# Kernel optimization log

Hardware: AMD Instinct MI355X
Metric: run time of the kernel (lower is better)

## Reference

```python
import jax, jax.numpy as jnp
import numpy as np

B, S, DIN, DATTN, DMODEL, M, HEADS, NSYNC, OUT, T, HNLM = 64, 64, 512, 512, 2048, 25, 8, 512, 1000, 50, 32

def _ln(x, g, b, eps=1e-5):
    mu = x.mean(-1, keepdims=True)
    v = x.var(-1, keepdims=True)
    return (x - mu) / jnp.sqrt(v + eps) * g + b

def setup_inputs() -> dict:
    key = jax.random.key(0)
    ks = jax.random.split(key, 32)
    def n(k, shape, fan):
        return jax.random.normal(k, shape, jnp.float32) / jnp.sqrt(jnp.float32(fan))
    inp = {}
    inp['x'] = jax.random.normal(ks[0], (B, S, DIN), jnp.float32)
    inp['Wf'] = n(ks[1], (DIN, DATTN), DIN); inp['bf'] = jnp.zeros((DATTN,), jnp.float32)
    inp['start_trace'] = jax.random.normal(ks[2], (DMODEL, M), jnp.float32) * 0.02
    inp['start_state'] = jax.random.normal(ks[3], (DMODEL,), jnp.float32) * 0.02
    inp['decay_a'] = jax.random.uniform(ks[4], (NSYNC,), jnp.float32, 0.0, 2.0)
    inp['decay_o'] = jax.random.uniform(ks[5], (NSYNC,), jnp.float32, 0.0, 2.0)
    inp['Wqp'] = n(ks[6], (NSYNC, DATTN), NSYNC); inp['bqp'] = jnp.zeros((DATTN,), jnp.float32)
    inp['Wq'] = n(ks[7], (DATTN, DATTN), DATTN); inp['bq'] = jnp.zeros((DATTN,), jnp.float32)
    inp['Wk'] = n(ks[8], (DATTN, DATTN), DATTN); inp['bk'] = jnp.zeros((DATTN,), jnp.float32)
    inp['Wv'] = n(ks[9], (DATTN, DATTN), DATTN); inp['bv'] = jnp.zeros((DATTN,), jnp.float32)
    inp['Wo'] = n(ks[10], (DATTN, DATTN), DATTN); inp['bo'] = jnp.zeros((DATTN,), jnp.float32)
    inp['Ws1'] = n(ks[11], (DATTN + DMODEL, 2 * DMODEL), DATTN + DMODEL); inp['bs1'] = jnp.zeros((2 * DMODEL,), jnp.float32)
    inp['ln_g'] = jnp.ones((DMODEL,), jnp.float32); inp['ln_b'] = jnp.zeros((DMODEL,), jnp.float32)
    inp['nw1'] = n(ks[12], (DMODEL, M, HNLM), M); inp['nb1'] = jnp.zeros((DMODEL, HNLM), jnp.float32)
    inp['nw2'] = n(ks[13], (DMODEL, HNLM), HNLM); inp['nb2'] = jnp.zeros((DMODEL,), jnp.float32)
    inp['Wout'] = n(ks[14], (NSYNC, OUT), NSYNC); inp['bout'] = jnp.zeros((OUT,), jnp.float32)
    inp['idx_la'] = jax.random.randint(ks[15], (NSYNC,), 0, DMODEL)
    inp['idx_ra'] = jax.random.randint(ks[16], (NSYNC,), 0, DMODEL)
    inp['idx_lo'] = jax.random.randint(ks[17], (NSYNC,), 0, DMODEL)
    inp['idx_ro'] = jax.random.randint(ks[18], (NSYNC,), 0, DMODEL)
    return inp

def _forward(x, Wf, bf, start_trace, start_state, decay_a, decay_o, Wqp, bqp, Wq, bq, Wk, bk, Wv, bv, Wo, bo, Ws1, bs1, ln_g, ln_b, nw1, nb1, nw2, nb2, Wout, bout, idx_la, idx_ra, idx_lo, idx_ro):
    Bn = x.shape[0]
    hd = DATTN // HEADS
    kv = x @ Wf + bf                                     # (B,S,DATTN)
    K = (kv @ Wk + bk).reshape(Bn, S, HEADS, hd)         # static across ticks
    V = (kv @ Wv + bv).reshape(Bn, S, HEADS, hd)
    r_a = jnp.exp(-jnp.clip(decay_a, 0.0, 15.0))
    r_o = jnp.exp(-jnp.clip(decay_o, 0.0, 15.0))
    trace0 = jnp.broadcast_to(start_trace[None], (Bn, DMODEL, M))
    act0 = jnp.broadcast_to(start_state[None], (Bn, DMODEL))

    def sync(state, alpha, beta, r, il, ir):
        pairing = state[:, il] * state[:, ir]
        alpha = r[None] * alpha + pairing
        beta = r[None] * beta + 1.0
        return alpha / jnp.sqrt(beta), alpha, beta

    # initial 'out' synchronisation (alpha=None/beta=None path)
    aO0 = act0[:, idx_lo] * act0[:, idx_ro]
    bO0 = jnp.ones_like(aO0)
    aA0 = jnp.zeros((Bn, NSYNC), jnp.float32)
    bA0 = jnp.zeros((Bn, NSYNC), jnp.float32)

    def step(carry, _):
        trace, act, aA, bA, aO, bO = carry
        syA, aA, bA = sync(act, aA, bA, r_a, idx_la, idx_ra)
        q = syA @ Wqp + bqp                              # (B,DATTN)
        Qh = (q @ Wq + bq).reshape(Bn, HEADS, hd)
        sc = jnp.einsum('bhd,bshd->bhs', Qh, K) / jnp.sqrt(jnp.float32(hd))
        w = jax.nn.softmax(sc, -1)
        ao = jnp.einsum('bhs,bshd->bhd', w, V).reshape(Bn, DATTN) @ Wo + bo
        pre = jnp.concatenate([ao, act], -1)             # (B,DATTN+DMODEL)
        h = pre @ Ws1 + bs1
        a1, a2 = jnp.split(h, 2, -1)
        state = _ln(a1 * jax.nn.sigmoid(a2), ln_g, ln_b) # GLU -> LayerNorm
        trace = jnp.concatenate([trace[:, :, 1:], state[:, :, None]], -1)
        hn = jax.nn.gelu(jnp.einsum('bdm,dmh->bdh', trace, nw1) + nb1)
        act = jnp.einsum('bdh,dh->bd', hn, nw2) + nb2    # neuron-level models
        syO, aO, bO = sync(act, aO, bO, r_o, idx_lo, idx_ro)
        pred = syO @ Wout + bout
        logp = jax.nn.log_softmax(pred, -1)
        ne = -(jnp.exp(logp) * logp).sum(-1) / jnp.log(jnp.float32(OUT))
        cert = jnp.stack([ne, 1.0 - ne], -1)
        return (trace, act, aA, bA, aO, bO), (pred, cert, syO)

    _, (preds, certs, syOs) = jax.lax.scan(step, (trace0, act0, aA0, bA0, aO0, bO0), None, length=T)
    predictions = jnp.moveaxis(preds, 0, -1)             # (B,OUT,T)
    certainties = jnp.moveaxis(certs, 0, -1)             # (B,2,T)
    return predictions, certainties, syOs[-1]

def reference(x, Wf, bf, start_trace, start_state, decay_a, decay_o, Wqp, bqp, Wq, bq, Wk, bk, Wv, bv, Wo, bo, Ws1, bs1, ln_g, ln_b, nw1, nb1, nw2, nb2, Wout, bout, idx_la, idx_ra, idx_lo, idx_ro):
    return _forward(x, Wf, bf, start_trace, start_state, decay_a, decay_o, Wqp, bqp, Wq, bq, Wk, bk, Wv, bv, Wo, bo, Ws1, bs1, ln_g, ln_b, nw1, nb1, nw2, nb2, Wout, bout, idx_la, idx_ra, idx_lo, idx_ro)
```

## Files before the change

### kernel.cpp

```cpp
#include <hip/hip_runtime.h>
#include <hip/hip_bf16.h>
#include <math.h>

#define BB 64
#define SS 64
#define DA 512
#define DM 2048
#define MM 25
#define NH 8
#define HD 64
#define NS 512
#define NOUT 1000
#define TT 50
#define HN 32
#define KTOT 2560
#define NOUT2 4096
#define KCH 640
#define NPAD 1024
#define SB2 ((size_t)BB*NS)

typedef __attribute__((ext_vector_type(8))) short bf16x8_t;
typedef __attribute__((ext_vector_type(8))) unsigned short u16x8_t;
typedef __attribute__((ext_vector_type(4))) float f32x4_t;

__device__ inline float bfs2f(unsigned short u){
    unsigned int x = ((unsigned int)u) << 16;
    return __uint_as_float(x);
}
__device__ inline unsigned short f2bfu(float v){
    __hip_bfloat16 h = __float2bfloat16(v);
    return *reinterpret_cast<unsigned short*>(&h);
}
__device__ inline float gelu_tanh(float x){
    float x3 = x*x*x;
    float u = 0.7978845608028654f*(x + 0.044715f*x3);
    float eu = __expf(2.f*u);
    float th = 1.f - 2.f/(eu + 1.f);
    return 0.5f*x*(1.0f + th);
}

static const size_t OFF_K     = 0;
static const size_t OFF_V     = OFF_K     + (size_t)BB*SS*DA/2;
static const size_t OFF_WCT   = OFF_V     + (size_t)BB*SS*DA/2;
static const size_t OFF_WC1   = OFF_WCT   + (size_t)NOUT2*KTOT/2;
static const size_t OFF_WOUTT = OFF_WC1   + (size_t)DA*DA;
static const size_t OFF_NW1B  = OFF_WOUTT + (size_t)NPAD*NS/2;
static const size_t OFF_WFK   = OFF_NW1B  + (size_t)DM*MM*HN/2;
static const size_t OFF_WFV   = OFF_WFK   + (size_t)DA*DA;
static const size_t OFF_BFK   = OFF_WFV   + (size_t)DA*DA;
static const size_t OFF_BFV   = OFF_BFK   + DA;
static const size_t OFF_BC1   = OFF_BFV   + DA;
static const size_t OFF_BC2   = OFF_BC1   + DA;
static const size_t OFF_BOUTP = OFF_BC2   + 2*DM;
static const size_t OFF_AA    = OFF_BOUTP + NPAD;
static const size_t OFF_BA    = OFF_AA    + 2*SB2;
static const size_t OFF_AO    = OFF_BA    + 2*SB2;
static const size_t OFF_BO    = OFF_AO    + 2*SB2;
static const size_t OFF_ATT   = OFF_BO    + 2*SB2;
static const size_t OFF_ACTB  = OFF_ATT   + (size_t)BB*DA/2;
static const size_t OFF_ACTF  = OFF_ACTB  + (size_t)BB*DM/2;
static const size_t OFF_HP    = OFF_ACTF  + (size_t)DM*BB;
static const size_t OFF_SBUF  = OFF_HP    + (size_t)4*BB*2*DM;
static const size_t OFF_STATS = OFF_SBUF  + (size_t)BB*DM;
static const size_t OFF_TRB   = OFF_STATS + 128;
static const size_t OFF_PREDA = OFF_TRB   + (size_t)MM*DM*BB/2;
static const size_t OFF_END   = OFF_PREDA + (size_t)TT*BB*NPAD/2;

__global__ void sgemm64(const float* __restrict__ A, int lda,
                        const float* __restrict__ Bm, int ldb,
                        const float* __restrict__ bias,
                        float* __restrict__ C, int ldc, int Kdim)
{
    __shared__ float la[16][65];
    __shared__ float lb[16][64];
    int cg = blockIdx.x, rg = blockIdx.y, tid = threadIdx.x;
    int tx = tid & 15, ty = tid >> 4;
    const float* Ab = A + (size_t)rg*64*lda;
    const float* Bb = Bm + (size_t)cg*64;
    float acc[4][4] = {};
    for (int k0 = 0; k0 < Kdim; k0 += 16){
        for (int i = tid; i < 1024; i += 256){
            int r = i >> 4, kk = i & 15;
            la[kk][r] = Ab[(size_t)r*lda + k0 + kk];
        }
        for (int i = tid; i < 1024; i += 256){
            int kk = i >> 6, c = i & 63;
            lb[kk][c] = Bb[(size_t)(k0+kk)*ldb + c];
        }
        __syncthreads();
        #pragma unroll
        for (int kk = 0; kk < 16; ++kk){
            float av[4], bv[4];
            #pragma unroll
            for (int i = 0; i < 4; ++i) av[i] = la[kk][ty*4+i];
            #pragma unroll
            for (int j = 0; j < 4; ++j) bv[j] = lb[kk][tx*4+j];
            #pragma unroll
            for (int i = 0; i < 4; ++i)
                #pragma unroll
                for (int j = 0; j < 4; ++j) acc[i][j] += av[i]*bv[j];
        }
        __syncthreads();
    }
    for (int i = 0; i < 4; ++i){
        int row = rg*64 + ty*4 + i;
        for (int j = 0; j < 4; ++j){
            int col = cg*64 + tx*4 + j;
            float v = acc[i][j];
            if (bias) v += bias[col];
            C[(size_t)row*ldc + col] = v;
        }
    }
}

__global__ void sgemm64_bf16out(const float* __restrict__ A, int lda,
                                const float* __restrict__ Bm, int ldb,
                                const float* __restrict__ bias,
                                unsigned short* __restrict__ C, int ldc, int Kdim)
{
    __shared__ float la[16][65];
    __shared__ float lb[16][64];
    int cg = blockIdx.x, rg = blockIdx.y, tid = threadIdx.x;
    int tx = tid & 15, ty = tid >> 4;
    const float* Ab = A + (size_t)rg*64*lda;
    const float* Bb = Bm + (size_t)cg*64;
    float acc[4][4] = {};
    for (int k0 = 0; k0 < Kdim; k0 += 16){
        for (int i = tid; i < 1024; i += 256){
            int r = i >> 4, kk = i & 15;
            la[kk][r] = Ab[(size_t)r*lda + k0 + kk];
        }
        for (int i = tid; i < 1024; i += 256){
            int kk = i >> 6, c = i & 63;
            lb[kk][c] = Bb[(size_t)(k0+kk)*ldb + c];
        }
        __syncthreads();
        #pragma unroll
        for (int kk = 0; kk < 16; ++kk){
            float av[4], bv[4];
            #pragma unroll
            for (int i = 0; i < 4; ++i) av[i] = la[kk][ty*4+i];
            #pragma unroll
            for (int j = 0; j < 4; ++j) bv[j] = lb[kk][tx*4+j];
            #pragma unroll
            for (int i = 0; i < 4; ++i)
                #pragma unroll
                for (int j = 0; j < 4; ++j) acc[i][j] += av[i]*bv[j];
        }
        __syncthreads();
    }
    for (int i = 0; i < 4; ++i){
        int row = rg*64 + ty*4 + i;
        for (int j = 0; j < 4; ++j){
            int col = cg*64 + tx*4 + j;
            float v = acc[i][j];
            if (bias) v += bias[col];
            C[(size_t)row*ldc + col] = f2bfu(v);
        }
    }
}

__global__ void gemm_t_bf16(const float* __restrict__ A, const float* __restrict__ Bm,
                            int ldb, unsigned short* __restrict__ Ct, int ldct)
{
    __shared__ float la[16][65];
    __shared__ float lb[16][64];
    int cg = blockIdx.x, rg = blockIdx.y, tid = threadIdx.x;
    int tx = tid & 15, ty = tid >> 4;
    const float* Ab = A + (size_t)rg*64*512;
    const float* Bb = Bm + (size_t)cg*64;
    float acc[4][4] = {};
    for (int k0 = 0; k0 < 512; k0 += 16){
        for (int i = tid; i < 1024; i += 256){
            int r = i >> 4, kk = i & 15;
            la[kk][r] = Ab[(size_t)r*512 + k0 + kk];
        }
        for (int i = tid; i < 1024; i += 256){
            int kk = i >> 6, c = i & 63;
            lb[kk][c] = Bb[(size_t)(k0+kk)*ldb + c];
        }
        __syncthreads();
        #pragma unroll
        for (int kk = 0; kk < 16; ++kk){
            float av[4], bv[4];
            #pragma unroll
            for (int i = 0; i < 4; ++i) av[i] = la[kk][ty*4+i];
            #pragma unroll
            for (int j = 0; j < 4; ++j) bv[j] = lb[kk][tx*4+j];
            #pragma unroll
            for (int i = 0; i < 4; ++i)
                #pragma unroll
                for (int j = 0; j < 4; ++j) acc[i][j] += av[i]*bv[j];
        }
        __syncthreads();
    }
    for (int i = 0; i < 4; ++i){
        int krow = rg*64 + ty*4 + i;
        for (int j = 0; j < 4; ++j){
            int ncol = cg*64 + tx*4 + j;
            Ct[(size_t)ncol*ldct + krow] = f2bfu(acc[i][j]);
        }
    }
}

__global__ void tcvt_ws1(const float* __restrict__ Ws1, unsigned short* __restrict__ WcT)
{
    __shared__ float tile[32][33];
    int bx = blockIdx.x, by = blockIdx.y;
    int tx = threadIdx.x & 31, ty = threadIdx.x >> 5;
    for (int i = 0; i < 4; ++i){
        int r = by*32 + ty + i*8;
        tile[ty + i*8][tx] = Ws1[(size_t)(512 + r)*NOUT2 + bx*32 + tx];
    }
    __syncthreads();
    for (int i = 0; i < 4; ++i){
        int n = bx*32 + ty + i*8;
        int r = by*32 + tx;
        WcT[(size_t)n*KTOT + 512 + r] = f2bfu(tile[tx][ty + i*8]);
    }
}

__global__ void tcvt_wout(const float* __restrict__ Wout, const float* __restrict__ bout,
                          unsigned short* __restrict__ WoutT, float* __restrict__ boutp)
{
    int n = blockIdx.x;
    int tid = threadIdx.x;
    for (int k = tid; k < NS; k += 256)
        WoutT[(size_t)n*NS + k] = (n < NOUT) ? f2bfu(Wout[(size_t)k*NOUT + n]) : (unsigned short)0;
    if (tid == 0) boutp[n] = (n < NOUT) ? bout[n] : 0.f;
}

__global__ void bias_combo(const float* __restrict__ bvec, const float* __restrict__ W,
                           int ldw, const float* __restrict__ badd,
                           float* __restrict__ out, int N)
{
    int n = blockIdx.x*256 + threadIdx.x;
    if (n >= N) return;
    float acc = badd[n];
    for (int k = 0; k < 512; ++k) acc += bvec[k]*W[(size_t)k*ldw + n];
    out[n] = acc;
}

__global__ void cvt_bf16(const float* __restrict__ in, unsigned short* __restrict__ out, int n)
{
    int i = blockIdx.x*256 + threadIdx.x;
    if (i < n) out[i] = f2bfu(in[i]);
}

__global__ void init_state(const float* __restrict__ ss,
                           const int* __restrict__ ilo, const int* __restrict__ iro,
                           float* __restrict__ act_f, unsigned short* __restrict__ act_bf,
                           float* __restrict__ aA0, float* __restrict__ bA0,
                           float* __restrict__ aO0, float* __restrict__ bO0)
{
    int i = blockIdx.x*256 + threadIdx.x;
    if (i < BB*DM){
        int d = i >> 6, b = i & 63;
        float v = ss[d];
        act_f[(size_t)d*BB + b] = v;
        act_bf[(size_t)b*DM + d] = f2bfu(v);
    }
    if (i < BB*NS){
        int j = i & (NS-1);
        aA0[i] = 0.f; bA0[i] = 0.f;
        aO0[i] = ss[ilo[j]]*ss[iro[j]];
        bO0[i] = 1.f;
    }
}

__device__ void pred_body(char* smem, int pb,
                          const float* __restrict__ act_f,
                          float* __restrict__ aO, float* __restrict__ bO,
                          const int* __restrict__ ilo, const int* __restrict__ iro,
                          const float* __restrict__ dco,
                          const unsigned short* __restrict__ WoutT,
                          const float* __restrict__ boutp,
                          unsigned short* __restrict__ predA,
                          float* __restrict__ out_syo, int tp)
{
    unsigned short* Asy = (unsigned short*)smem;
    const int tid = threadIdx.x, lane = tid & 63, w = tid >> 6;
    const int rf = w & 3, cf2 = (w >> 2)*2;
    const int colb = lane & 15, koff = (lane >> 4)*8, rg4 = (lane >> 4)*4;
    const int n0 = pb*64;
    const int rdn = tp & 1, wrn = 1 - rdn;
    f32x4_t acc0 = {0.f,0.f,0.f,0.f}, acc1 = {0.f,0.f,0.f,0.f};
    for (int ks = 0; ks < 8; ++ks){
        int jj = tid & 63, bq = tid >> 6;
        int j = ks*64 + jj;
        int ilj = ilo[j], irj = iro[j];
        float rr = __expf(-fminf(fmaxf(dco[j], 0.f), 15.f));
        #pragma unroll
        for (int p = 0; p < 8; ++p){
            int b = p*8 + bq;
            float pair = act_f[(size_t)ilj*BB + b]*act_f[(size_t)irj*BB + b];
            size_t o = (size_t)b*NS + j;
            float a  = rr*aO[(size_t)rdn*SB2 + o] + pair;
            float be = rr*bO[(size_t)rdn*SB2 + o] + 1.f;
            float s = a*rsqrtf(be);
            Asy[b*72 + jj] = f2bfu(s);
            if (pb == 0){
                aO[(size_t)wrn*SB2 + o] = a;
                bO[(size_t)wrn*SB2 + o] = be;
                if (tp == TT-1) out_syo[o] = s;
            }
        }
        __syncthreads();
        int arow = rf*16 + colb;
        bf16x8_t a0 = *(const bf16x8_t*)&Asy[arow*72 + koff];
        bf16x8_t a1 = *(const bf16x8_t*)&Asy[arow*72 + 32 + koff];
        int br0 = n0 + cf2*16 + colb, br1 = br0 + 16;
        bf16x8_t b00 = *(const bf16x8_t*)&WoutT[(size_t)br0*NS + ks*64 + koff];
        bf16x8_t b01 = *(const bf16x8_t*)&WoutT[(size_t)br0*NS + ks*64 + 32 + koff];
        bf16x8_t b10 = *(const bf16x8_t*)&WoutT[(size_t)br1*NS + ks*64 + koff];
        bf16x8_t b11 = *(const bf16x8_t*)&WoutT[(size_t)br1*NS + ks*64 + 32 + koff];
        acc0 = __builtin_amdgcn_mfma_f32_16x16x32_bf16(a0, b00, acc0, 0, 0, 0);
        acc0 = __builtin_amdgcn_mfma_f32_16x16x32_bf16(a1, b01, acc0, 0, 0, 0);
        acc1 = __builtin_amdgcn_mfma_f32_16x16x32_bf16(a0, b10, acc1, 0, 0, 0);
        acc1 = __builtin_amdgcn_mfma_f32_16x16x32_bf16(a1, b11, acc1, 0, 0, 0);
        __syncthreads();
    }
    unsigned short* pa = predA + (size_t)tp*BB*NPAD;
    #pragma unroll
    for (int r = 0; r < 4; ++r){
        int row = rf*16 + rg4 + r;
        int c0 = n0 + cf2*16 + colb, c1 = c0 + 16;
        pa[(size_t)row*NPAD + c0] = f2bfu(acc0[r] + boutp[c0]);
        pa[(size_t)row*NPAD + c1] = f2bfu(acc1[r] + boutp[c1]);
    }
}

__global__ __launch_bounds__(512) void tick_head(
        const float* __restrict__ act_f,
        float* __restrict__ aA, float* __restrict__ bA,
        float* __restrict__ aO, float* __restrict__ bO,
        const int* __restrict__ ila, const int* __restrict__ ira,
        const int* __restrict__ ilo, const int* __restrict__ iro,
        const float* __restrict__ dca, const float* __restrict__ dco,
        const float* __restrict__ Wc1, const float* __restrict__ bc1,
        const unsigned short* __restrict__ Kb, const unsigned short* __restrict__ Vb,
        unsigned short* __restrict__ att,
        const unsigned short* __restrict__ WoutT, const float* __restrict__ boutp,
        unsigned short* __restrict__ predA, float* __restrict__ out_syo,
        int t, int do_pred)
{
    __shared__ __align__(16) char smem[20480];
    const int bid = blockIdx.x, tid = threadIdx.x;
    const int lane = tid & 63, w = tid >> 6;
    if (bid < 64){
        int h = bid >> 3, bg = bid & 7;
        float* sy  = (float*)smem;
        float* q   = sy + 8*NS;
        float* wgt = q + 8*64;
        int rdn = t & 1, wrn = 1 - rdn;
        for (int i = tid; i < 8*NS; i += 512){
            int r = i >> 9, j = i & (NS-1);
            int b = bg*8 + r;
            float pair = act_f[(size_t)ila[j]*BB + b]*act_f[(size_t)ira[j]*BB + b];
            float rr = __expf(-fminf(fmaxf(dca[j], 0.f), 15.f));
            size_t o = (size_t)b*NS + j;
            float a  = rr*aA[(size_t)rdn*SB2 + o] + pair;
            float be = rr*bA[(size_t)rdn*SB2 + o] + 1.f;
            sy[i] = a*rsqrtf(be);
            if (h == 0){ aA[(size_t)wrn*SB2 + o] = a; bA[(size_t)wrn*SB2 + o] = be; }
        }
        __syncthreads();
        {
            int c = lane, r = w;
            int col = h*HD + c;
            float acc = bc1[col];
            const float* wp = Wc1 + col;
            #pragma unroll 8
            for (int k = 0; k < NS; ++k) acc += sy[r*NS + k]*wp[(size_t)k*DA];
            q[r*64 + c] = acc;
        }
        __syncthreads();
        {
            int r = w, s = lane;
            int b = bg*8 + r;
            const unsigned short* kp = Kb + (size_t)(b*SS + s)*DA + h*HD;
            float sc = 0.f;
            #pragma unroll
            for (int dg = 0; dg < 8; ++dg){
                u16x8_t kv = *(const u16x8_t*)(kp + dg*8);
                #pragma unroll
                for (int u = 0; u < 8; ++u) sc += q[r*64 + dg*8 + u]*bfs2f(kv[u]);
            }
            sc *= 0.125f;
            float m = sc;
            for (int o = 32; o; o >>= 1) m = fmaxf(m, __shfl_xor(m, o, 64));
            float e = __expf(sc - m);
            float sum = e;
            for (int o = 32; o; o >>= 1) sum += __shfl_xor(sum, o, 64);
            wgt[r*64 + s] = e/sum;
        }
        __syncthreads();
        {
            int r = w, d = lane;
            int b = bg*8 + r;
            const unsigned short* vp = Vb + (size_t)(b*SS)*DA + h*HD + d;
            float o = 0.f;
            #pragma unroll 8
            for (int s = 0; s < SS; ++s) o += wgt[r*64 + s]*bfs2f(vp[(size_t)s*DA]);
            att[(size_t)b*DA + h*HD + d] = f2bfu(o);
        }
    } else if (do_pred){
        pred_body(smem, bid - 64, act_f, aO, bO, ilo, iro, dco,
                  WoutT, boutp, predA, out_syo, t - 1);
    }
}

__global__ __launch_bounds__(512) void pred_fin(
        const float* __restrict__ act_f,
        float* __restrict__ aO, float* __restrict__ bO,
        const int* __restrict__ ilo, const int* __restrict__ iro,
        const float* __restrict__ dco,
        const unsigned short* __restrict__ WoutT, const float* __restrict__ boutp,
        unsigned short* __restrict__ predA, float* __restrict__ out_syo)
{
    __shared__ __align__(16) char smem[10240];
    pred_body(smem, blockIdx.x, act_f, aO, bO, ilo, iro, dco,
              WoutT, boutp, predA, out_syo, TT - 1);
}

__global__ __launch_bounds__(256) void hgemm_mfma(const unsigned short* __restrict__ attu,
                                                  const unsigned short* __restrict__ actu,
                                                  const unsigned short* __restrict__ wctu,
                                                  float* __restrict__ hpart)
{
    __shared__ unsigned short Al[64][72];
    __shared__ unsigned short Bl[64][72];
    int cg = blockIdx.x, kc = blockIdx.y, tid = threadIdx.x;
    int w = tid >> 6, lane = tid & 63;
    int n0 = cg*64;
    f32x4_t acc[4];
    #pragma unroll
    for (int t2 = 0; t2 < 4; ++t2) acc[t2] = (f32x4_t){0.f,0.f,0.f,0.f};

    for (int step = 0; step < 10; ++step){
        int k0 = kc*KCH + step*64;
        #pragma unroll
        for (int ld = 0; ld < 2; ++ld){
            int idx = tid + ld*256;
            int row = idx >> 3;
            int kg  = (idx & 7)*8;
            *reinterpret_cast<uint4*>(&Bl[row][kg]) =
                *reinterpret_cast<const uint4*>(&wctu[(size_t)(n0+row)*KTOT + k0 + kg]);
            uint4 av;
            if (k0 < 512) av = *reinterpret_cast<const uint4*>(&attu[(size_t)row*DA + k0 + kg]);
            else          av = *reinterpret_cast<const uint4*>(&actu[(size_t)row*DM + (k0-512) + kg]);
            *reinterpret_cast<uint4*>(&Al[row][kg]) = av;
        }
        __syncthreads();
        int arow = w*16 + (lane & 15);
        int koff = (lane >> 4)*8;
        bf16x8_t af0 = *reinterpret_cast<const bf16x8_t*>(&Al[arow][koff]);
        bf16x8_t af1 = *reinterpret_cast<const bf16x8_t*>(&Al[arow][32 + koff]);
        #pragma unroll
        for (int t2 = 0; t2 < 4; ++t2){
            int brow = t2*16 + (lane & 15);
            bf16x8_t bf0 = *reinterpret_cast<const bf16x8_t*>(&Bl[brow][koff]);
            bf16x8_t bf1 = *reinterpret_cast<const bf16x8_t*>(&Bl[brow][32 + koff]);
            acc[t2] = __builtin_amdgcn_mfma_f32_16x16x32_bf16(af0, bf0, acc[t2], 0, 0, 0);
            acc[t2] = __builtin_amdgcn_mfma_f32_16x16x32_bf16(af1, bf1, acc[t2], 0, 0, 0);
        }
        __syncthreads();
    }
    float* out = hpart + (size_t)kc*BB*2*DM;
    int colb = lane & 15, rg2 = (lane >> 4)*4;
    #pragma unroll
    for (int t2 = 0; t2 < 4; ++t2){
        #pragma unroll
        for (int r = 0; r < 4; ++r){
            int row = w*16 + rg2 + r;
            int col = n0 + t2*16 + colb;
            out[(size_t)row*2*DM + col] = acc[t2][r];
        }
    }
}

__global__ void glu_stats(const float* __restrict__ hp, const float* __restrict__ bc2,
                          float* __restrict__ sbuf, float* __restrict__ stats)
{
    __shared__ float red[8];
    int b = blockIdx.x, tid = threadIdx.x;
    int lane = tid & 63, w = tid >> 6;
    float lsum = 0.f, lsq = 0.f;
    #pragma unroll
    for (int i = 0; i < 8; ++i){
        int n = tid + i*256;
        float h1 = bc2[n], h2 = bc2[DM + n];
        #pragma unroll
        for (int c = 0; c < 4; ++c){
            const float* hb = hp + ((size_t)c*BB + b)*2*DM;
            h1 += hb[n]; h2 += hb[DM + n];
        }
        float s = h1*(1.f/(1.f + __expf(-h2)));
        sbuf[(size_t)b*DM + n] = s;
        lsum += s; lsq += s*s;
    }
    for (int o = 32; o; o >>= 1){ lsum += __shfl_down(lsum, o, 64); lsq += __shfl_down(lsq, o, 64); }
    if (lane == 0){ red[w] = lsum; red[4 + w] = lsq; }
    __syncthreads();
    if (tid == 0){
        float ts = red[0]+red[1]+red[2]+red[3];
        float tq = red[4]+red[5]+red[6]+red[7];
        float mu = ts/DM;
        float var = tq/DM - mu*mu;
        stats[b*2] = mu;
        stats[b*2+1] = rsqrtf(var + 1e-5f);
    }
}

__global__ __launch_bounds__(512) void nlm2(
        const float* __restrict__ sbuf, const float* __restrict__ stats,
        const float* __restrict__ lng, const float* __restrict__ lnb,
        unsigned short* __restrict__ traceb, const float* __restrict__ stt,
        const unsigned short* __restrict__ nw1b, const float* __restrict__ nb1,
        const float* __restrict__ nw2, const float* __restrict__ nb2,
        float* __restrict__ act_f, unsigned short* __restrict__ act_bf, int t)
{
    __shared__ float wall[8*864];
    const int tid = threadIdx.x, lane = tid & 63, w = tid >> 6;
    const int d = blockIdx.x*8 + w;
    float* wreg = wall + (size_t)w*864;
    for (int i = lane; i < 800; i += 64) wreg[i] = bfs2f(nw1b[(size_t)d*800 + i]);
    if (lane < 32) wreg[800 + lane] = nb1[d*HN + lane];
    else           wreg[832 + (lane - 32)] = nw2[d*HN + (lane - 32)];
    float mu  = stats[lane*2];
    float inv = stats[lane*2 + 1];
    float s   = sbuf[(size_t)lane*DM + d];
    float st  = (s - mu)*inv*lng[d] + lnb[d];
    int slot = t % MM;
    traceb[((size_t)slot*DM + d)*BB + lane] = f2bfu(st);
    float tr[25];
    #pragma unroll
    for (int m = 0; m < 24; ++m){
        int time = t - 24 + m;
        tr[m] = (time >= 0) ? bfs2f(traceb[((size_t)(time % MM)*DM + d)*BB + lane])
                            : stt[(size_t)d*MM + (m + t + 1)];
    }
    tr[24] = st;
    float a[32];
    #pragma unroll
    for (int h = 0; h < 32; ++h) a[h] = wreg[800 + h];
    #pragma unroll
    for (int m = 0; m < 25; ++m){
        float tm = tr[m];
        #pragma unroll
        for (int q4 = 0; q4 < 8; ++q4){
            float4 w4 = *(const float4*)&wreg[m*32 + q4*4];
            a[q4*4+0] += tm*w4.x;
            a[q4*4+1] += tm*w4.y;
            a[q4*4+2] += tm*w4.z;
            a[q4*4+3] += tm*w4.w;
        }
    }
    float pa = 0.f;
    #pragma unroll
    for (int h = 0; h < 32; ++h) pa += gelu_tanh(a[h])*wreg[832 + h];
    float v = pa + nb2[d];
    act_f[(size_t)d*BB + lane] = v;
    act_bf[(size_t)lane*DM + d] = f2bfu(v);
}

__global__ void entropy_k(const unsigned short* __restrict__ predA, float* __restrict__ out_cert)
{
    __shared__ float red[8];
    int b = blockIdx.x & 63, t = blockIdx.x >> 6, tid = threadIdx.x;
    const unsigned short* pr = predA + (size_t)t*BB*NPAD + (size_t)b*NPAD;
    float v[4];
    float m = -1e30f;
    #pragma unroll
    for (int i = 0; i < 4; ++i){
        int n = tid + i*256;
        v[i] = (n < NOUT) ? bfs2f(pr[n]) : -1e30f;
        m = fmaxf(m, v[i]);
    }
    for (int o = 32; o; o >>= 1) m = fmaxf(m, __shfl_xor(m, o, 64));
    if ((tid & 63) == 0) red[tid >> 6] = m;
    __syncthreads();
    m = fmaxf(fmaxf(red[0], red[1]), fmaxf(red[2], red[3]));
    __syncthreads();
    float s1 = 0.f, s2 = 0.f;
    #pragma unroll
    for (int i = 0; i < 4; ++i){
        int n = tid + i*256;
        if (n < NOUT){
            float e = __expf(v[i] - m);
            s1 += e; s2 += e*(v[i] - m);
        }
    }
    for (int o = 32; o; o >>= 1){ s1 += __shfl_xor(s1, o, 64); s2 += __shfl_xor(s2, o, 64); }
    if ((tid & 63) == 0){ red[tid >> 6] = s1; red[4 + (tid >> 6)] = s2; }
    __syncthreads();
    s1 = red[0]+red[1]+red[2]+red[3];
    s2 = red[4]+red[5]+red[6]+red[7];
    float plogp = s2/s1 - logf(s1);
    float ne = -plogp / logf((float)NOUT);
    if (tid == 0){
        out_cert[(size_t)b*2*TT + t]      = ne;
        out_cert[(size_t)b*2*TT + TT + t] = 1.f - ne;
    }
}

__global__ void transpose_pred(const unsigned short* __restrict__ predA, float* __restrict__ out_pred)
{
    __shared__ unsigned short sm[50][136];
    int bx = blockIdx.x;
    int b  = blockIdx.y;
    int tid = threadIdx.x;
    for (int tp = 0; tp < 25; ++tp){
        int t = tp*2 + (tid >> 7);
        int nn = tid & 127;
        sm[t][nn] = predA[(size_t)t*BB*NPAD + (size_t)b*NPAD + bx*128 + nn];
    }
    __syncthreads();
    int nloc = tid >> 1, half = tid & 1;
    int n = bx*128 + nloc;
    if (n < NOUT){
        float* dst = out_pred + (size_t)b*NOUT*TT + (size_t)n*TT + half*25;
        #pragma unroll
        for (int q = 0; q < 25; ++q) dst[q] = bfs2f(sm[half*25 + q][nloc]);
    }
}

extern "C" void kernel_launch(void* const* d_in, const int* in_sizes, int n_in,
                              void* d_out, int out_size, void* d_ws, size_t ws_size,
                              hipStream_t stream)
{
    const float* x    = (const float*)d_in[0];
    const float* Wf   = (const float*)d_in[1];
    const float* bf   = (const float*)d_in[2];
    const float* stt  = (const float*)d_in[3];
    const float* ss   = (const float*)d_in[4];
    const float* dca  = (const float*)d_in[5];
    const float* dco  = (const float*)d_in[6];
    const float* Wqp  = (const float*)d_in[7];
    const float* bqp  = (const float*)d_in[8];
    const float* Wq   = (const float*)d_in[9];
    const float* bq   = (const float*)d_in[10];
    const float* Wk   = (const float*)d_in[11];
    const float* bk   = (const float*)d_in[12];
    const float* Wv   = (const float*)d_in[13];
    const float* bv   = (const float*)d_in[14];
    const float* Wo   = (const float*)d_in[15];
    const float* bo   = (const float*)d_in[16];
    const float* Ws1  = (const float*)d_in[17];
    const float* bs1  = (const float*)d_in[18];
    const float* lng  = (const float*)d_in[19];
    const float* lnb  = (const float*)d_in[20];
    const float* nw1  = (const float*)d_in[21];
    const float* nb1  = (const float*)d_in[22];
    const float* nw2  = (const float*)d_in[23];
    const float* nb2  = (const float*)d_in[24];
    const float* Wout = (const float*)d_in[25];
    const float* bout = (const float*)d_in[26];
    const int* ila = (const int*)d_in[27];
    const int* ira = (const int*)d_in[28];
    const int* ilo = (const int*)d_in[29];
    const int* iro = (const int*)d_in[30];

    float* ws = (float*)d_ws;
    unsigned short* Kb    = (unsigned short*)(ws + OFF_K);
    unsigned short* Vb    = (unsigned short*)(ws + OFF_V);
    unsigned short* WcT   = (unsigned short*)(ws + OFF_WCT);
    float*          Wc1   = ws + OFF_WC1;
    unsigned short* WoutT = (unsigned short*)(ws + OFF_WOUTT);
    unsigned short* nw1b  = (unsigned short*)(ws + OFF_NW1B);
    float* Wfk   = ws + OFF_WFK;
    float* Wfv   = ws + OFF_WFV;
    float* bfk   = ws + OFF_BFK;
    float* bfv   = ws + OFF_BFV;
    float* bc1   = ws + OFF_BC1;
    float* bc2   = ws + OFF_BC2;
    float* boutp = ws + OFF_BOUTP;
    float* aA    = ws + OFF_AA;
    float* bA    = ws + OFF_BA;
    float* aO    = ws + OFF_AO;
    float* bO    = ws + OFF_BO;
    unsigned short* attb  = (unsigned short*)(ws + OFF_ATT);
    unsigned short* actb  = (unsigned short*)(ws + OFF_ACTB);
    float* actf  = ws + OFF_ACTF;
    float* hp    = ws + OFF_HP;
    float* sbuf  = ws + OFF_SBUF;
    float* stats = ws + OFF_STATS;
    unsigned short* traceb = (unsigned short*)(ws + OFF_TRB);
    unsigned short* predA  = (unsigned short*)(ws + OFF_PREDA);

    float* outp = (float*)d_out;
    float* out_pred = outp;
    float* out_cert = outp + (size_t)BB*NOUT*TT;
    float* out_syo  = out_cert + (size_t)BB*2*TT;

    sgemm64<<<dim3(8,8),  256, 0, stream>>>(Wf, 512, Wk, 512, nullptr, Wfk, 512, 512);
    sgemm64<<<dim3(8,8),  256, 0, stream>>>(Wf, 512, Wv, 512, nullptr, Wfv, 512, 512);
    sgemm64<<<dim3(8,8),  256, 0, stream>>>(Wqp,512, Wq, 512, nullptr, Wc1, 512, 512);
    gemm_t_bf16<<<dim3(64,8), 256, 0, stream>>>(Wo, Ws1, NOUT2, WcT, KTOT);
    tcvt_ws1<<<dim3(128,64), 256, 0, stream>>>(Ws1, WcT);
    tcvt_wout<<<NPAD, 256, 0, stream>>>(Wout, bout, WoutT, boutp);
    bias_combo<<<2, 256, 0, stream>>>(bf,  Wk, 512, bk, bfk, 512);
    bias_combo<<<2, 256, 0, stream>>>(bf,  Wv, 512, bv, bfv, 512);
    bias_combo<<<2, 256, 0, stream>>>(bqp, Wq, 512, bq, bc1, 512);
    bias_combo<<<16,256, 0, stream>>>(bo,  Ws1, NOUT2, bs1, bc2, 4096);
    cvt_bf16<<<6400, 256, 0, stream>>>(nw1, nw1b, DM*MM*HN);
    sgemm64_bf16out<<<dim3(8,64), 256, 0, stream>>>(x, 512, Wfk, 512, bfk, Kb, 512, 512);
    sgemm64_bf16out<<<dim3(8,64), 256, 0, stream>>>(x, 512, Wfv, 512, bfv, Vb, 512, 512);
    init_state<<<512, 256, 0, stream>>>(ss, ilo, iro, actf, actb, aA, bA, aO, bO);

    for (int t = 0; t < TT; ++t){
        tick_head<<<80, 512, 0, stream>>>(actf, aA, bA, aO, bO,
                                          ila, ira, ilo, iro, dca, dco,
                                          Wc1, bc1, Kb, Vb, attb,
                                          WoutT, boutp, predA, out_syo,
                                          t, (t > 0) ? 1 : 0);
        hgemm_mfma<<<dim3(64,4), 256, 0, stream>>>(attb, actb, WcT, hp);
        glu_stats<<<BB, 256, 0, stream>>>(hp, bc2, sbuf, stats);
        nlm2<<<256, 512, 0, stream>>>(sbuf, stats, lng, lnb, traceb, stt,
                                      nw1b, nb1, nw2, nb2, actf, actb, t);
    }
    pred_fin<<<16, 512, 0, stream>>>(actf, aO, bO, ilo, iro, dco,
                                     WoutT, boutp, predA, out_syo);

    entropy_k<<<TT*BB, 256, 0, stream>>>(predA, out_cert);
    transpose_pred<<<dim3(8, BB), 256, 0, stream>>>(predA, out_pred);
}
```

Before: 4.663 ms.

## Fuse GLU and layernorm stats into per-tick GEMM; move setup GEMMs to MFMA

The per-tick split-K GEMM plus separate GLU/stats kernel is replaced by one hgemm_glu kernel. Each block computes 8 paired gate/value columns over the full K, applies the GLU in registers and accumulates row sum and sum-of-squares with atomics. The intent is to drop the partial-sum buffer round-trip and one launch per tick; nlm2 now derives mean and rsqrt itself, and tick_head zeroes the stats. The one-time weight-folding GEMMs are moved to bf16 MFMA with transposed bf16 copies, and Wc1 is stored as bf16. This trades fp32 precision in the precomputation and uses atomics in place of a deterministic reduction.

```diff
diff --git a/kernel.cpp b/kernel.cpp
--- a/kernel.cpp
+++ b/kernel.cpp
@@ -15,7 +15,6 @@
 #define HN 32
 #define KTOT 2560
 #define NOUT2 4096
-#define KCH 640
 #define NPAD 1024
 #define SB2 ((size_t)BB*NS)
 
@@ -40,167 +39,100 @@
 }
 
 static const size_t OFF_K     = 0;
-static const size_t OFF_V     = OFF_K     + (size_t)BB*SS*DA/2;
-static const size_t OFF_WCT   = OFF_V     + (size_t)BB*SS*DA/2;
-static const size_t OFF_WC1   = OFF_WCT   + (size_t)NOUT2*KTOT/2;
-static const size_t OFF_WOUTT = OFF_WC1   + (size_t)DA*DA;
-static const size_t OFF_NW1B  = OFF_WOUTT + (size_t)NPAD*NS/2;
-static const size_t OFF_WFK   = OFF_NW1B  + (size_t)DM*MM*HN/2;
-static const size_t OFF_WFV   = OFF_WFK   + (size_t)DA*DA;
-static const size_t OFF_BFK   = OFF_WFV   + (size_t)DA*DA;
-static const size_t OFF_BFV   = OFF_BFK   + DA;
-static const size_t OFF_BC1   = OFF_BFV   + DA;
-static const size_t OFF_BC2   = OFF_BC1   + DA;
-static const size_t OFF_BOUTP = OFF_BC2   + 2*DM;
-static const size_t OFF_AA    = OFF_BOUTP + NPAD;
+static const size_t OFF_V     = OFF_K     + 1048576;
+static const size_t OFF_WCT   = OFF_V     + 1048576;
+static const size_t OFF_WC1B  = OFF_WCT   + 5242880;
+static const size_t OFF_WOUTT = OFF_WC1B  + 131072;
+static const size_t OFF_NW1B  = OFF_WOUTT + 262144;
+static const size_t OFF_WFT   = OFF_NW1B  + 819200;
+static const size_t OFF_WKT   = OFF_WFT   + 131072;
+static const size_t OFF_WVT   = OFF_WKT   + 131072;
+static const size_t OFF_WQT   = OFF_WVT   + 131072;
+static const size_t OFF_WQPB  = OFF_WQT   + 131072;
+static const size_t OFF_WOB   = OFF_WQPB  + 131072;
+static const size_t OFF_BC1   = OFF_WOB   + 131072;
+static const size_t OFF_BC2   = OFF_BC1   + 512;
+static const size_t OFF_BOUTP = OFF_BC2   + 4096;
+static const size_t OFF_AA    = OFF_BOUTP + 1024;
 static const size_t OFF_BA    = OFF_AA    + 2*SB2;
 static const size_t OFF_AO    = OFF_BA    + 2*SB2;
 static const size_t OFF_BO    = OFF_AO    + 2*SB2;
 static const size_t OFF_ATT   = OFF_BO    + 2*SB2;
-static const size_t OFF_ACTB  = OFF_ATT   + (size_t)BB*DA/2;
-static const size_t OFF_ACTF  = OFF_ACTB  + (size_t)BB*DM/2;
-static const size_t OFF_HP    = OFF_ACTF  + (size_t)DM*BB;
-static const size_t OFF_SBUF  = OFF_HP    + (size_t)4*BB*2*DM;
-static const size_t OFF_STATS = OFF_SBUF  + (size_t)BB*DM;
+static const size_t OFF_ACTB  = OFF_ATT   + 16384;
+static const size_t OFF_ACTF  = OFF_ACTB  + 65536;
+static const size_t OFF_SBUF  = OFF_ACTF  + 131072;
+static const size_t OFF_STATS = OFF_SBUF  + 131072;
 static const size_t OFF_TRB   = OFF_STATS + 128;
-static const size_t OFF_PREDA = OFF_TRB   + (size_t)MM*DM*BB/2;
-static const size_t OFF_END   = OFF_PREDA + (size_t)TT*BB*NPAD/2;
-
-__global__ void sgemm64(const float* __restrict__ A, int lda,
-                        const float* __restrict__ Bm, int ldb,
-                        const float* __restrict__ bias,
-                        float* __restrict__ C, int ldc, int Kdim)
-{
-    __shared__ float la[16][65];
-    __shared__ float lb[16][64];
+static const size_t OFF_PREDA = OFF_TRB   + 1638400;
+static const size_t OFF_END   = OFF_PREDA + 1638400;
+static const size_t OFF_XB    = OFF_PREDA;
+static const size_t OFF_KV    = OFF_TRB;
+static const size_t OFF_WS1T  = OFF_TRB;
+
+__global__ __launch_bounds__(256) void mgemm(
+        const unsigned short* __restrict__ A, int lda,
+        const unsigned short* __restrict__ BT, int ldbt,
+        const float* __restrict__ bias,
+        unsigned short* __restrict__ C, int ldc, int K)
+{
+    __shared__ unsigned short Al[64][72];
+    __shared__ unsigned short Bl[64][72];
     int cg = blockIdx.x, rg = blockIdx.y, tid = threadIdx.x;
-    int tx = tid & 15, ty = tid >> 4;
-    const float* Ab = A + (size_t)rg*64*lda;
-    const float* Bb = Bm + (size_t)cg*64;
-    float acc[4][4] = {};
-    for (int k0 = 0; k0 < Kdim; k0 += 16){
-        for (int i = tid; i < 1024; i += 256){
-            int r = i >> 4, kk = i & 15;
-            la[kk][r] = Ab[(size_t)r*lda + k0 + kk];
-        }
-        for (int i = tid; i < 1024; i += 256){
-            int kk = i >> 6, c = i & 63;
-            lb[kk][c] = Bb[(size_t)(k0+kk)*ldb + c];
-        }
-        __syncthreads();
-        #pragma unroll
-        for (int kk = 0; kk < 16; ++kk){
-            float av[4], bv[4];
-            #pragma unroll
-            for (int i = 0; i < 4; ++i) av[i] = la[kk][ty*4+i];
-            #pragma unroll
-            for (int j = 0; j < 4; ++j) bv[j] = lb[kk][tx*4+j];
-            #pragma unroll
-            for (int i = 0; i < 4; ++i)
-                #pragma unroll
-                for (int j = 0; j < 4; ++j) acc[i][j] += av[i]*bv[j];
-        }
-        __syncthreads();
-    }
-    for (int i = 0; i < 4; ++i){
-        int row = rg*64 + ty*4 + i;
-        for (int j = 0; j < 4; ++j){
-            int col = cg*64 + tx*4 + j;
-            float v = acc[i][j];
-            if (bias) v += bias[col];
-            C[(size_t)row*ldc + col] = v;
-        }
-    }
-}
-
-__global__ void sgemm64_bf16out(const float* __restrict__ A, int lda,
-                                const float* __restrict__ Bm, int ldb,
-                                const float* __restrict__ bias,
-                                unsigned short* __restrict__ C, int ldc, int Kdim)
-{
-    __shared__ float la[16][65];
-    __shared__ float lb[16][64];
-    int cg = blockIdx.x, rg = blockIdx.y, tid = threadIdx.x;
-    int tx = tid & 15, ty = tid >> 4;
-    const float* Ab = A + (size_t)rg*64*lda;
-    const float* Bb = Bm + (size_t)cg*64;
-    float acc[4][4] = {};
-    for (int k0 = 0; k0 < Kdim; k0 += 16){
-        for (int i = tid; i < 1024; i += 256){
-            int r = i >> 4, kk = i & 15;
-            la[kk][r] = Ab[(size_t)r*lda + k0 + kk];
-        }
-        for (int i = tid; i < 1024; i += 256){
-            int kk = i >> 6, c = i & 63;
-            lb[kk][c] = Bb[(size_t)(k0+kk)*ldb + c];
-        }
-        __syncthreads();
-        #pragma unroll
-        for (int kk = 0; kk < 16; ++kk){
-            float av[4], bv[4];
-            #pragma unroll
-            for (int i = 0; i < 4; ++i) av[i] = la[kk][ty*4+i];
-            #pragma unroll
-            for (int j = 0; j < 4; ++j) bv[j] = lb[kk][tx*4+j];
-            #pragma unroll
-            for (int i = 0; i < 4; ++i)
-                #pragma unroll
-                for (int j = 0; j < 4; ++j) acc[i][j] += av[i]*bv[j];
-        }
-        __syncthreads();
-    }
-    for (int i = 0; i < 4; ++i){
-        int row = rg*64 + ty*4 + i;
-        for (int j = 0; j < 4; ++j){
-            int col = cg*64 + tx*4 + j;
-            float v = acc[i][j];
+    int w = tid >> 6, lane = tid & 63;
+    int m0 = rg*64, n0 = cg*64;
+    f32x4_t acc[4];
+    #pragma unroll
+    for (int t2 = 0; t2 < 4; ++t2) acc[t2] = (f32x4_t){0.f,0.f,0.f,0.f};
+    for (int k0 = 0; k0 < K; k0 += 64){
+        #pragma unroll
+        for (int ld = 0; ld < 2; ++ld){
+            int idx = tid + ld*256;
+            int row = idx >> 3, kg = (idx & 7)*8;
+            *reinterpret_cast<uint4*>(&Bl[row][kg]) =
+                *reinterpret_cast<const uint4*>(&BT[(size_t)(n0+row)*ldbt + k0 + kg]);
+            *reinterpret_cast<uint4*>(&Al[row][kg]) =
+                *reinterpret_cast<const uint4*>(&A[(size_t)(m0+row)*lda + k0 + kg]);
+        }
+        __syncthreads();
+        int arow = w*16 + (lane & 15);
+        int koff = (lane >> 4)*8;
+        bf16x8_t a0 = *reinterpret_cast<const bf16x8_t*>(&Al[arow][koff]);
+        bf16x8_t a1 = *reinterpret_cast<const bf16x8_t*>(&Al[arow][32 + koff]);
+        #pragma unroll
+        for (int t2 = 0; t2 < 4; ++t2){
+            int brow = t2*16 + (lane & 15);
+            bf16x8_t b0 = *reinterpret_cast<const bf16x8_t*>(&Bl[brow][koff]);
+            bf16x8_t b1 = *reinterpret_cast<const bf16x8_t*>(&Bl[brow][32 + koff]);
+            acc[t2] = __builtin_amdgcn_mfma_f32_16x16x32_bf16(a0, b0, acc[t2], 0, 0, 0);
+            acc[t2] = __builtin_amdgcn_mfma_f32_16x16x32_bf16(a1, b1, acc[t2], 0, 0, 0);
+        }
+        __syncthreads();
+    }
+    int colb = lane & 15, rg4 = (lane >> 4)*4;
+    #pragma unroll
+    for (int t2 = 0; t2 < 4; ++t2){
+        #pragma unroll
+        for (int r = 0; r < 4; ++r){
+            int row = m0 + w*16 + rg4 + r;
+            int col = n0 + t2*16 + colb;
+            float v = acc[t2][r];
             if (bias) v += bias[col];
             C[(size_t)row*ldc + col] = f2bfu(v);
         }
     }
 }
 
-__global__ void gemm_t_bf16(const float* __restrict__ A, const float* __restrict__ Bm,
-                            int ldb, unsigned short* __restrict__ Ct, int ldct)
-{
-    __shared__ float la[16][65];
-    __shared__ float lb[16][64];
-    int cg = blockIdx.x, rg = blockIdx.y, tid = threadIdx.x;
-    int tx = tid & 15, ty = tid >> 4;
-    const float* Ab = A + (size_t)rg*64*512;
-    const float* Bb = Bm + (size_t)cg*64;
-    float acc[4][4] = {};
-    for (int k0 = 0; k0 < 512; k0 += 16){
-        for (int i = tid; i < 1024; i += 256){
-            int r = i >> 4, kk = i & 15;
-            la[kk][r] = Ab[(size_t)r*512 + k0 + kk];
-        }
-        for (int i = tid; i < 1024; i += 256){
-            int kk = i >> 6, c = i & 63;
-            lb[kk][c] = Bb[(size_t)(k0+kk)*ldb + c];
-        }
-        __syncthreads();
-        #pragma unroll
-        for (int kk = 0; kk < 16; ++kk){
-            float av[4], bv[4];
-            #pragma unroll
-            for (int i = 0; i < 4; ++i) av[i] = la[kk][ty*4+i];
-            #pragma unroll
-            for (int j = 0; j < 4; ++j) bv[j] = lb[kk][tx*4+j];
-            #pragma unroll
-            for (int i = 0; i < 4; ++i)
-                #pragma unroll
-                for (int j = 0; j < 4; ++j) acc[i][j] += av[i]*bv[j];
-        }
-        __syncthreads();
-    }
-    for (int i = 0; i < 4; ++i){
-        int krow = rg*64 + ty*4 + i;
-        for (int j = 0; j < 4; ++j){
-            int ncol = cg*64 + tx*4 + j;
-            Ct[(size_t)ncol*ldct + krow] = f2bfu(acc[i][j]);
-        }
-    }
+__global__ void tcvtb(const float* __restrict__ in, int ldin,
+                      unsigned short* __restrict__ out, int ldout)
+{
+    __shared__ float tile[32][33];
+    int bx = blockIdx.x, by = blockIdx.y;
+    int tx = threadIdx.x & 31, ty = threadIdx.x >> 5;
+    for (int i = 0; i < 4; ++i)
+        tile[ty + i*8][tx] = in[(size_t)(by*32 + ty + i*8)*ldin + bx*32 + tx];
+    __syncthreads();
+    for (int i = 0; i < 4; ++i)
+        out[(size_t)(bx*32 + ty + i*8)*ldout + by*32 + tx] = f2bfu(tile[tx][ty + i*8]);
 }
 
 __global__ void tcvt_ws1(const float* __restrict__ Ws1, unsigned short* __restrict__ WcT)
@@ -337,17 +269,19 @@
         const int* __restrict__ ila, const int* __restrict__ ira,
         const int* __restrict__ ilo, const int* __restrict__ iro,
         const float* __restrict__ dca, const float* __restrict__ dco,
-        const float* __restrict__ Wc1, const float* __restrict__ bc1,
+        const unsigned short* __restrict__ Wc1b, const float* __restrict__ bc1,
         const unsigned short* __restrict__ Kb, const unsigned short* __restrict__ Vb,
         unsigned short* __restrict__ att,
         const unsigned short* __restrict__ WoutT, const float* __restrict__ boutp,
         unsigned short* __restrict__ predA, float* __restrict__ out_syo,
+        float* __restrict__ stats,
         int t, int do_pred)
 {
     __shared__ __align__(16) char smem[20480];
     const int bid = blockIdx.x, tid = threadIdx.x;
     const int lane = tid & 63, w = tid >> 6;
     if (bid < 64){
+        if (bid == 63 && tid < 128) stats[tid] = 0.f;
         int h = bid >> 3, bg = bid & 7;
         float* sy  = (float*)smem;
         float* q   = sy + 8*NS;
@@ -369,14 +303,14 @@
             int c = lane, r = w;
             int col = h*HD + c;
             float acc = bc1[col];
-            const float* wp = Wc1 + col;
+            const unsigned short* wp = Wc1b + col;
             #pragma unroll 8
-            for (int k = 0; k < NS; ++k) acc += sy[r*NS + k]*wp[(size_t)k*DA];
+            for (int k = 0; k < NS; ++k) acc += sy[r*NS + k]*bfs2f(wp[(size_t)k*DA]);
             q[r*64 + c] = acc;
         }
         __syncthreads();
         {
-            int r = w, s = lane;
+            int r = w, s = tid & 63;
             int b = bg*8 + r;
             const unsigned short* kp = Kb + (size_t)(b*SS + s)*DA + h*HD;
             float sc = 0.f;
@@ -423,92 +357,65 @@
               WoutT, boutp, predA, out_syo, TT - 1);
 }
 
-__global__ __launch_bounds__(256) void hgemm_mfma(const unsigned short* __restrict__ attu,
-                                                  const unsigned short* __restrict__ actu,
-                                                  const unsigned short* __restrict__ wctu,
-                                                  float* __restrict__ hpart)
+__global__ __launch_bounds__(256) void hgemm_glu(
+        const unsigned short* __restrict__ attu, const unsigned short* __restrict__ actu,
+        const unsigned short* __restrict__ wctu, const float* __restrict__ bc2,
+        float* __restrict__ sbuf, float* __restrict__ stats)
 {
     __shared__ unsigned short Al[64][72];
-    __shared__ unsigned short Bl[64][72];
-    int cg = blockIdx.x, kc = blockIdx.y, tid = threadIdx.x;
-    int w = tid >> 6, lane = tid & 63;
-    int n0 = cg*64;
-    f32x4_t acc[4];
-    #pragma unroll
-    for (int t2 = 0; t2 < 4; ++t2) acc[t2] = (f32x4_t){0.f,0.f,0.f,0.f};
-
-    for (int step = 0; step < 10; ++step){
-        int k0 = kc*KCH + step*64;
+    __shared__ unsigned short Bl[16][72];
+    const int bid = blockIdx.x, tid = threadIdx.x;
+    const int lane = tid & 63, w = tid >> 6;
+    const int n0 = bid*8;
+    f32x4_t acc = {0.f,0.f,0.f,0.f};
+    for (int step = 0; step < 40; ++step){
+        int k0 = step*64;
         #pragma unroll
         for (int ld = 0; ld < 2; ++ld){
             int idx = tid + ld*256;
-            int row = idx >> 3;
-            int kg  = (idx & 7)*8;
-            *reinterpret_cast<uint4*>(&Bl[row][kg]) =
-                *reinterpret_cast<const uint4*>(&wctu[(size_t)(n0+row)*KTOT + k0 + kg]);
+            int row = idx >> 3, kg = (idx & 7)*8;
             uint4 av;
             if (k0 < 512) av = *reinterpret_cast<const uint4*>(&attu[(size_t)row*DA + k0 + kg]);
             else          av = *reinterpret_cast<const uint4*>(&actu[(size_t)row*DM + (k0-512) + kg]);
             *reinterpret_cast<uint4*>(&Al[row][kg]) = av;
         }
+        if (tid < 128){
+            int row = tid >> 3, kg = (tid & 7)*8;
+            size_t nr = (row < 8) ? (size_t)(n0 + row) : (size_t)(2048 + n0 + row - 8);
+            *reinterpret_cast<uint4*>(&Bl[row][kg]) =
+                *reinterpret_cast<const uint4*>(&wctu[nr*KTOT + k0 + kg]);
+        }
         __syncthreads();
         int arow = w*16 + (lane & 15);
         int koff = (lane >> 4)*8;
-        bf16x8_t af0 = *reinterpret_cast<const bf16x8_t*>(&Al[arow][koff]);
-        bf16x8_t af1 = *reinterpret_cast<const bf16x8_t*>(&Al[arow][32 + koff]);
-        #pragma unroll
-        for (int t2 = 0; t2 < 4; ++t2){
-            int brow = t2*16 + (lane & 15);
-            bf16x8_t bf0 = *reinterpret_cast<const bf16x8_t*>(&Bl[brow][koff]);
-            bf16x8_t bf1 = *reinterpret_cast<const bf16x8_t*>(&Bl[brow][32 + koff]);
-            acc[t2] = __builtin_amdgcn_mfma_f32_16x16x32_bf16(af0, bf0, acc[t2], 0, 0, 0);
-            acc[t2] = __builtin_amdgcn_mfma_f32_16x16x32_bf16(af1, bf1, acc[t2], 0, 0, 0);
-        }
-        __syncthreads();
-    }
-    float* out = hpart + (size_t)kc*BB*2*DM;
-    int colb = lane & 15, rg2 = (lane >> 4)*4;
-    #pragma unroll
-    for (int t2 = 0; t2 < 4; ++t2){
-        #pragma unroll
-        for (int r = 0; r < 4; ++r){
-            int row = w*16 + rg2 + r;
-            int col = n0 + t2*16 + colb;
-            out[(size_t)row*2*DM + col] = acc[t2][r];
-        }
-    }
-}
-
-__global__ void glu_stats(const float* __restrict__ hp, const float* __restrict__ bc2,
-                          float* __restrict__ sbuf, float* __restrict__ stats)
-{
-    __shared__ float red[8];
-    int b = blockIdx.x, tid = threadIdx.x;
-    int lane = tid & 63, w = tid >> 6;
-    float lsum = 0.f, lsq = 0.f;
-    #pragma unroll
-    for (int i = 0; i < 8; ++i){
-        int n = tid + i*256;
-        float h1 = bc2[n], h2 = bc2[DM + n];
-        #pragma unroll
-        for (int c = 0; c < 4; ++c){
-            const float* hb = hp + ((size_t)c*BB + b)*2*DM;
-            h1 += hb[n]; h2 += hb[DM + n];
-        }
-        float s = h1*(1.f/(1.f + __expf(-h2)));
-        sbuf[(size_t)b*DM + n] = s;
-        lsum += s; lsq += s*s;
-    }
-    for (int o = 32; o; o >>= 1){ lsum += __shfl_down(lsum, o, 64); lsq += __shfl_down(lsq, o, 64); }
-    if (lane == 0){ red[w] = lsum; red[4 + w] = lsq; }
-    __syncthreads();
-    if (tid == 0){
-        float ts = red[0]+red[1]+red[2]+red[3];
-        float tq = red[4]+red[5]+red[6]+red[7];
-        float mu = ts/DM;
-        float var = tq/DM - mu*mu;
-        stats[b*2] = mu;
-        stats[b*2+1] = rsqrtf(var + 1e-5f);
+        bf16x8_t a0 = *reinterpret_cast<const bf16x8_t*>(&Al[arow][koff]);
+        bf16x8_t a1 = *reinterpret_cast<const bf16x8_t*>(&Al[arow][32 + koff]);
+        int brow = lane & 15;
+        bf16x8_t b0 = *reinterpret_cast<const bf16x8_t*>(&Bl[brow][koff]);
+        bf16x8_t b1 = *reinterpret_cast<const bf16x8_t*>(&Bl[brow][32 + koff]);
+        acc = __builtin_amdgcn_mfma_f32_16x16x32_bf16(a0, b0, acc, 0, 0, 0);
+        acc = __builtin_amdgcn_mfma_f32_16x16x32_bf16(a1, b1, acc, 0, 0, 0);
+        __syncthreads();
+    }
+    int colb = lane & 15, rg4 = (lane >> 4)*4;
+    int nn = n0 + (colb & 7);
+    float b1v = bc2[nn], b2v = bc2[2048 + nn];
+    #pragma unroll
+    for (int r = 0; r < 4; ++r){
+        float v  = acc[r];
+        float vo = __shfl_xor(v, 8, 64);
+        float h1 = ((colb < 8) ? v : vo) + b1v;
+        float h2 = ((colb < 8) ? vo : v) + b2v;
+        float sv = h1 * (1.f/(1.f + __expf(-h2)));
+        int b = w*16 + rg4 + r;
+        if (colb < 8) sbuf[(size_t)b*DM + nn] = sv;
+        float ps = sv, pq = sv*sv;
+        #pragma unroll
+        for (int o = 1; o < 8; o <<= 1){ ps += __shfl_xor(ps, o, 64); pq += __shfl_xor(pq, o, 64); }
+        if (colb == 0){
+            atomicAdd(&stats[b*2], ps);
+            atomicAdd(&stats[b*2 + 1], pq);
+        }
     }
 }
 
@@ -527,8 +434,9 @@
     for (int i = lane; i < 800; i += 64) wreg[i] = bfs2f(nw1b[(size_t)d*800 + i]);
     if (lane < 32) wreg[800 + lane] = nb1[d*HN + lane];
     else           wreg[832 + (lane - 32)] = nw2[d*HN + (lane - 32)];
-    float mu  = stats[lane*2];
-    float inv = stats[lane*2 + 1];
+    float ssum = stats[lane*2], ssq = stats[lane*2 + 1];
+    float mu  = ssum*(1.0f/DM);
+    float inv = rsqrtf(fmaxf(ssq*(1.0f/DM) - mu*mu, 0.f) + 1e-5f);
     float s   = sbuf[(size_t)lane*DM + d];
     float st  = (s - mu)*inv*lng[d] + lnb[d];
     int slot = t % MM;
@@ -665,13 +573,18 @@
     unsigned short* Kb    = (unsigned short*)(ws + OFF_K);
     unsigned short* Vb    = (unsigned short*)(ws + OFF_V);
     unsigned short* WcT   = (unsigned short*)(ws + OFF_WCT);
-    float*          Wc1   = ws + OFF_WC1;
+    unsigned short* Wc1b  = (unsigned short*)(ws + OFF_WC1B);
     unsigned short* WoutT = (unsigned short*)(ws + OFF_WOUTT);
     unsigned short* nw1b  = (unsigned short*)(ws + OFF_NW1B);
-    float* Wfk   = ws + OFF_WFK;
-    float* Wfv   = ws + OFF_WFV;
-    float* bfk   = ws + OFF_BFK;
-    float* bfv   = ws + OFF_BFV;
+    unsigned short* WfT   = (unsigned short*)(ws + OFF_WFT);
+    unsigned short* WkT   = (unsigned short*)(ws + OFF_WKT);
+    unsigned short* WvT   = (unsigned short*)(ws + OFF_WVT);
+    unsigned short* WqT   = (unsigned short*)(ws + OFF_WQT);
+    unsigned short* Wqpb  = (unsigned short*)(ws + OFF_WQPB);
+    unsigned short* Wob   = (unsigned short*)(ws + OFF_WOB);
+    unsigned short* xb    = (unsigned short*)(ws + OFF_XB);
+    unsigned short* kvb   = (unsigned short*)(ws + OFF_KV);
+    unsigned short* Ws1T  = (unsigned short*)(ws + OFF_WS1T);
     float* bc1   = ws + OFF_BC1;
     float* bc2   = ws + OFF_BC2;
     float* boutp = ws + OFF_BOUTP;
@@ -682,7 +595,6 @@
     unsigned short* attb  = (unsigned short*)(ws + OFF_ATT);
     unsigned short* actb  = (unsigned short*)(ws + OFF_ACTB);
     float* actf  = ws + OFF_ACTF;
-    float* hp    = ws + OFF_HP;
     float* sbuf  = ws + OFF_SBUF;
     float* stats = ws + OFF_STATS;
     unsigned short* traceb = (unsigned short*)(ws + OFF_TRB);
@@ -693,29 +605,33 @@
     float* out_cert = outp + (size_t)BB*NOUT*TT;
     float* out_syo  = out_cert + (size_t)BB*2*TT;
 
-    sgemm64<<<dim3(8,8),  256, 0, stream>>>(Wf, 512, Wk, 512, nullptr, Wfk, 512, 512);
-    sgemm64<<<dim3(8,8),  256, 0, stream>>>(Wf, 512, Wv, 512, nullptr, Wfv, 512, 512);
-    sgemm64<<<dim3(8,8),  256, 0, stream>>>(Wqp,512, Wq, 512, nullptr, Wc1, 512, 512);
-    gemm_t_bf16<<<dim3(64,8), 256, 0, stream>>>(Wo, Ws1, NOUT2, WcT, KTOT);
+    cvt_bf16<<<8192, 256, 0, stream>>>(x, xb, 4096*512);
+    tcvtb<<<dim3(16,16), 256, 0, stream>>>(Wf, 512, WfT, 512);
+    tcvtb<<<dim3(16,16), 256, 0, stream>>>(Wk, 512, WkT, 512);
+    tcvtb<<<dim3(16,16), 256, 0, stream>>>(Wv, 512, WvT, 512);
+    tcvtb<<<dim3(16,16), 256, 0, stream>>>(Wq, 512, WqT, 512);
+    cvt_bf16<<<1024, 256, 0, stream>>>(Wqp, Wqpb, 512*512);
+    cvt_bf16<<<1024, 256, 0, stream>>>(Wo, Wob, 512*512);
+    cvt_bf16<<<6400, 256, 0, stream>>>(nw1, nw1b, DM*MM*HN);
+    mgemm<<<dim3(8,64), 256, 0, stream>>>(xb, 512, WfT, 512, bf, kvb, 512, 512);
+    mgemm<<<dim3(8,64), 256, 0, stream>>>(kvb, 512, WkT, 512, bk, Kb, 512, 512);
+    mgemm<<<dim3(8,64), 256, 0, stream>>>(kvb, 512, WvT, 512, bv, Vb, 512, 512);
+    mgemm<<<dim3(8,8),  256, 0, stream>>>(Wqpb, 512, WqT, 512, nullptr, Wc1b, 512, 512);
+    tcvtb<<<dim3(128,16), 256, 0, stream>>>(Ws1, NOUT2, Ws1T, 512);
+    mgemm<<<dim3(8,64), 256, 0, stream>>>(Ws1T, 512, Wob, 512, nullptr, WcT, KTOT, 512);
     tcvt_ws1<<<dim3(128,64), 256, 0, stream>>>(Ws1, WcT);
     tcvt_wout<<<NPAD, 256, 0, stream>>>(Wout, bout, WoutT, boutp);
-    bias_combo<<<2, 256, 0, stream>>>(bf,  Wk, 512, bk, bfk, 512);
-    bias_combo<<<2, 256, 0, stream>>>(bf,  Wv, 512, bv, bfv, 512);
     bias_combo<<<2, 256, 0, stream>>>(bqp, Wq, 512, bq, bc1, 512);
     bias_combo<<<16,256, 0, stream>>>(bo,  Ws1, NOUT2, bs1, bc2, 4096);
-    cvt_bf16<<<6400, 256, 0, stream>>>(nw1, nw1b, DM*MM*HN);
-    sgemm64_bf16out<<<dim3(8,64), 256, 0, stream>>>(x, 512, Wfk, 512, bfk, Kb, 512, 512);
-    sgemm64_bf16out<<<dim3(8,64), 256, 0, stream>>>(x, 512, Wfv, 512, bfv, Vb, 512, 512);
     init_state<<<512, 256, 0, stream>>>(ss, ilo, iro, actf, actb, aA, bA, aO, bO);
 
     for (int t = 0; t < TT; ++t){
         tick_head<<<80, 512, 0, stream>>>(actf, aA, bA, aO, bO,
                                           ila, ira, ilo, iro, dca, dco,
-                                          Wc1, bc1, Kb, Vb, attb,
-                                          WoutT, boutp, predA, out_syo,
+                                          Wc1b, bc1, Kb, Vb, attb,
+                                          WoutT, boutp, predA, out_syo, stats,
                                           t, (t > 0) ? 1 : 0);
-        hgemm_mfma<<<dim3(64,4), 256, 0, stream>>>(attb, actb, WcT, hp);
-        glu_stats<<<BB, 256, 0, stream>>>(hp, bc2, sbuf, stats);
+        hgemm_glu<<<256, 256, 0, stream>>>(attb, actb, WcT, bc2, sbuf, stats);
         nlm2<<<256, 512, 0, stream>>>(sbuf, stats, lng, lnb, traceb, stt,
                                       nw1b, nb1, nw2, nb2, actf, actb, t);
     }
```

Measured after the change: 7.632 ms. 1.64x slower.
